# Kernel tuning notes

Hardware: AMD Instinct MI355X
Metric: run time of the kernel (lower is better)

## Reference

```python
import jax, jax.numpy as jnp
import numpy as np

VARIANCES = (0.1, 0.2)
THRESHOLD = 0.35
NEG_POS = 7
NUM_CLASSES = 3
B, P, G = 64, 32768, 64


def point_form(boxes):
    # (cx,cy,w,h) -> (x1,y1,x2,y2)
    return jnp.concatenate([boxes[:, :2] - boxes[:, 2:] / 2,
                            boxes[:, :2] + boxes[:, 2:] / 2], axis=1)


def jaccard(a, b):
    # a: [G,4], b: [P,4], both point-form -> IoU [G,P]
    lt = jnp.maximum(a[:, None, :2], b[None, :, :2])
    rb = jnp.minimum(a[:, None, 2:], b[None, :, 2:])
    wh = jnp.clip(rb - lt, 0.0)
    inter = wh[..., 0] * wh[..., 1]
    area_a = (a[:, 2] - a[:, 0]) * (a[:, 3] - a[:, 1])
    area_b = (b[:, 2] - b[:, 0]) * (b[:, 3] - b[:, 1])
    return inter / (area_a[:, None] + area_b[None, :] - inter)


def encode(matched, priors):
    # matched point-form [P,4], priors center-form [P,4]
    g_cxcy = ((matched[:, :2] + matched[:, 2:]) / 2 - priors[:, :2]) / (VARIANCES[0] * priors[:, 2:])
    g_wh = jnp.log((matched[:, 2:] - matched[:, :2]) / priors[:, 2:]) / VARIANCES[1]
    return jnp.concatenate([g_cxcy, g_wh], axis=1)


def encode_landm(matched, priors):
    # matched [P,10] -> [P,5,2] offsets
    m = matched.reshape(-1, 5, 2)
    g = (m - priors[:, None, :2]) / (VARIANCES[0] * priors[:, None, 2:])
    return g.reshape(-1, 10)


def match_one(truths, labels, landms, priors, priors_pt):
    overlaps = jaccard(truths, priors_pt)                     # [G,P]
    best_prior_overlap = overlaps.max(axis=1)                 # [G]
    best_prior_idx = overlaps.argmax(axis=1)                  # [G]
    valid_gt = best_prior_overlap >= 0.2                      # filter hard gt
    any_valid = valid_gt.any()
    best_truth_overlap = overlaps.max(axis=0)                 # [P]
    best_truth_idx = overlaps.argmax(axis=0)                  # [P]
    # force-match: each valid gt claims its best prior (overlap set to 2 > threshold)
    best_truth_overlap = best_truth_overlap.at[best_prior_idx].max(jnp.where(valid_gt, 2.0, -1.0))
    best_truth_idx = best_truth_idx.at[best_prior_idx].set(jnp.arange(truths.shape[0]))
    matches = truths[best_truth_idx]                          # [P,4]
    conf = labels[best_truth_idx].astype(jnp.int32)           # [P]
    conf = jnp.where(best_truth_overlap < THRESHOLD, 0, conf)
    loc = encode(matches, priors)
    landm = encode_landm(landms[best_truth_idx], priors)
    # early-return branch of match(): no valid gt -> loc_t = 0, conf_t = 0
    loc = jnp.where(any_valid, loc, 0.0)
    conf = jnp.where(any_valid, conf, 0)
    return loc, conf, landm


def smooth_l1(d):
    ad = jnp.abs(d)
    return jnp.where(ad < 1.0, 0.5 * d * d, ad - 0.5)


def setup_inputs() -> dict:
    key = jax.random.key(0)
    k1, k2, k3, k4, k5, k6, k7, k8 = jax.random.split(key, 8)
    loc_data = jax.random.normal(k1, (B, P, 4), dtype=jnp.float32)
    conf_data = jax.random.normal(k2, (B, P, NUM_CLASSES), dtype=jnp.float32)
    landm_data = jax.random.normal(k3, (B, P, 10), dtype=jnp.float32)
    # priors: center-form, in (0,1)
    cxcy = jax.random.uniform(k4, (P, 2), dtype=jnp.float32)
    pwh = jax.random.uniform(k5, (P, 2), dtype=jnp.float32) * 0.28 + 0.02
    priors = jnp.concatenate([cxcy, pwh], axis=1)
    # targets: [B,G,15] = 4 box (point-form) + 10 landm + 1 label in {1,2}
    x1y1 = jax.random.uniform(k6, (B, G, 2), dtype=jnp.float32) * 0.8
    twh = jax.random.uniform(k7, (B, G, 2), dtype=jnp.float32) * 0.18 + 0.02
    lm = jax.random.uniform(k8, (B, G, 10), dtype=jnp.float32)
    lbl = jax.random.randint(jax.random.fold_in(key, 9), (B, G, 1), 1, 3).astype(jnp.float32)
    targets = jnp.concatenate([x1y1, x1y1 + twh, lm, lbl], axis=2)
    return {"loc_data": loc_data, "conf_data": conf_data, "landm_data": landm_data,
            "priors": priors, "targets": targets}


def reference(loc_data, conf_data, landm_data, priors, targets):
    num, num_priors = loc_data.shape[0], priors.shape[0]
    priors_pt = point_form(priors)
    truths, landms, labels = targets[:, :, :4], targets[:, :, 4:14], targets[:, :, 14]
    loc_t, conf_t, landm_t = jax.vmap(match_one, in_axes=(0, 0, 0, None, None))(
        truths, labels, landms, priors, priors_pt)
    loc_t = jax.lax.stop_gradient(loc_t)      # torch builds targets from .data
    landm_t = jax.lax.stop_gradient(landm_t)
    f32 = jnp.float32
    # ---- landmark loss (face: all 10 coords; mask: first 4 coords only) ----
    N1 = jnp.maximum((conf_t > 0).sum().astype(f32), 1.0)
    face = (conf_t == 1)[..., None]
    maskc = (conf_t == 2)[..., None]
    el = smooth_l1(landm_data - landm_t)                      # [B,P,10]
    loss_landm = (el * face).sum() + (el[..., :4] * maskc).sum()
    # ---- localization loss over all positives ----
    pos = conf_t != 0
    loss_l = (smooth_l1(loc_data - loc_t) * pos[..., None]).sum()
    # ---- hard negative mining + confidence loss ----
    conf_t2 = jnp.where(conf_t < 0, 1, conf_t)                # no-landmark faces -> class 1
    lse = jax.nn.logsumexp(conf_data, axis=-1)                # [B,P]
    gathered = jnp.take_along_axis(conf_data, conf_t2[..., None], axis=-1)[..., 0]
    loss_c = jnp.where(pos, 0.0, lse - gathered)              # [B,P]
    loss_idx = jnp.argsort(-loss_c, axis=1)                   # sort descending
    idx_rank = jnp.argsort(loss_idx, axis=1)                  # rank of each prior
    num_pos = pos.sum(axis=1, keepdims=True)
    num_neg = jnp.minimum(NEG_POS * num_pos, num_priors - 1)
    neg = idx_rank < num_neg
    sel = pos | neg
    loss_c_final = jnp.where(sel, lse - gathered, 0.0).sum()
    N = jnp.maximum(num_pos.sum().astype(f32), 1.0)
    return (loss_l / N, loss_c_final / N, loss_landm / N1)
```

## Files before the change

kernel.cpp:

```cpp
#include <hip/hip_runtime.h>

#define B 64
#define P 32768
#define G 64


__device__ __forceinline__ float sl1(float d) {
    float ad = fabsf(d);
    return (ad < 1.0f) ? 0.5f * d * d : (ad - 0.5f);
}

__global__ void k0_init(const float* __restrict__ targets, float* __restrict__ truth_pre,
                        unsigned long long* __restrict__ bp_packed,
                        int* __restrict__ num_pos, int* __restrict__ any_valid,
                        double* __restrict__ acc) {
    int i = blockIdx.x * 256 + threadIdx.x;
    if (i < B * G) {
        const float* t = targets + (size_t)i * 15;
        float x1 = t[0], y1 = t[1], x2 = t[2], y2 = t[3];
        float* o = truth_pre + (size_t)i * 8;
        o[0] = x1; o[1] = y1; o[2] = x2; o[3] = y2;
        o[4] = (x2 - x1) * (y2 - y1); o[5] = t[14]; o[6] = 0.f; o[7] = 0.f;
        bp_packed[i] = 0ull;
    }
    if (i < B) { num_pos[i] = 0; any_valid[i] = 0; }
    if (i < 8) acc[i] = 0.0;
}

__launch_bounds__(256, 8)
__global__ void k1_match(const float* __restrict__ priors, const float* __restrict__ truth_pre,
                         float* __restrict__ bto, int* __restrict__ bti,
                         unsigned long long* __restrict__ bp_packed) {
    __shared__ unsigned long long lbp[G];
    int b = blockIdx.y, tid = threadIdx.x;
    int lane = tid & 63;
    int p = blockIdx.x * 256 + tid;
    int pbase_wave = blockIdx.x * 256 + (tid & ~63);

    float4 pr = ((const float4*)priors)[p];
    float px1 = pr.x - pr.z * 0.5f, py1 = pr.y - pr.w * 0.5f;
    float px2 = pr.x + pr.z * 0.5f, py2 = pr.y + pr.w * 0.5f;
    float pa = (px2 - px1) * (py2 - py1);

    if (tid < G) lbp[tid] = 0ull;
    __syncthreads();

    float bestv = 0.f;
    int bestg = 0;
    const float* tb = truth_pre + (size_t)b * G * 8;

#pragma unroll 4
    for (int g = 0; g < G; ++g) {
        const float* t = tb + g * 8;
        float lx = fmaxf(px1, t[0]);
        float ly = fmaxf(py1, t[1]);
        float rx = fminf(px2, t[2]);
        float ry = fminf(py2, t[3]);
        float w = fmaxf(rx - lx, 0.f), h = fmaxf(ry - ly, 0.f);
        float inter = w * h;
        float denom = (pa + t[4]) - inter;
        float iou = inter * __builtin_amdgcn_rcpf(denom);
        bool better = iou > bestv;
        bestv = better ? iou : bestv;
        bestg = better ? g : bestg;
        float m = iou;
#pragma unroll
        for (int off = 1; off < 64; off <<= 1) m = fmaxf(m, __shfl_xor(m, off));
        unsigned long long msk = __ballot(iou == m);
        int src = __ffsll((long long)msk) - 1;
        unsigned long long pk = ((unsigned long long)__float_as_uint(m) << 32)
                              | (unsigned int)~(unsigned int)(pbase_wave + src);
        if (lane == 0) atomicMax(&lbp[g], pk);
    }
    __syncthreads();
    if (tid < G) atomicMax(&bp_packed[b * G + tid], lbp[tid]);
    bto[(size_t)b * P + p] = bestv;
    bti[(size_t)b * P + p] = bestg;
}

__global__ void k2_force(const unsigned long long* __restrict__ bp_packed,
                         float* __restrict__ bto, int* __restrict__ bti,
                         int* __restrict__ any_valid) {
    int b = blockIdx.x, g = threadIdx.x;
    unsigned long long pk = bp_packed[b * G + g];
    float bpo = __uint_as_float((unsigned int)(pk >> 32));
    unsigned int bpi = ~((unsigned int)pk);
    bool valid = bpo >= 0.2f;
    unsigned long long ball = __ballot(valid);
    if (g == 0) any_valid[b] = (ball != 0ull) ? 1 : 0;
    if (valid) bto[(size_t)b * P + bpi] = 2.0f;
    atomicMax(&bti[(size_t)b * P + bpi], 256 + g);
}

__launch_bounds__(256, 4)
__global__ void k3_loss(const float* __restrict__ loc_data, const float* __restrict__ conf_data,
                        const float* __restrict__ landm_data, const float* __restrict__ priors,
                        const float* __restrict__ targets,
                        const float* __restrict__ bto, const int* __restrict__ bti,
                        const int* __restrict__ any_valid,
                        float* __restrict__ c_neg, int* __restrict__ num_pos,
                        float4* __restrict__ part3) {
    __shared__ float st[G * 15];
    __shared__ float rbuf[12];
    __shared__ int ribuf[4];
    int b = blockIdx.y, tid = threadIdx.x;
    int p = blockIdx.x * 256 + tid;
    for (int i = tid; i < G * 15; i += 256) st[i] = targets[(size_t)b * G * 15 + i];
    __syncthreads();

    size_t idx = (size_t)b * P + p;
    int v = bti[idx];
    int g = (v >= 256) ? (v - 256) : v;
    float ov = bto[idx];
    int conf = 0;
    if (any_valid[b] != 0 && ov >= 0.35f) conf = (int)st[g * 15 + 14];

    const float* cd = conf_data + idx * 3;
    float c0 = cd[0], c1 = cd[1], c2 = cd[2];
    float m = fmaxf(c0, fmaxf(c1, c2));
    float lse = m + __logf(__expf(c0 - m) + __expf(c1 - m) + __expf(c2 - m));
    float gath = (conf == 0) ? c0 : ((conf == 1) ? c1 : c2);
    float lc = lse - gath;

    float cn = 0.f, lloss = 0.f, lmloss = 0.f, plse = 0.f;
    int np = 0;
    if (conf != 0) { np = 1; plse = lc; }
    else cn = fmaxf(lc, 0.f);
    c_neg[idx] = cn;

    if (conf != 0) {
        float4 pr = ((const float4*)priors)[p];
        const float* t = st + g * 15;
        float t0 = t[0], t1 = t[1], t2 = t[2], t3 = t[3];
        float gcx = ((t0 + t2) * 0.5f - pr.x) / (0.1f * pr.z);
        float gcy = ((t1 + t3) * 0.5f - pr.y) / (0.1f * pr.w);
        float gw = __logf((t2 - t0) / pr.z) / 0.2f;
        float gh = __logf((t3 - t1) / pr.w) / 0.2f;
        float4 ld = ((const float4*)loc_data)[idx];
        lloss = sl1(ld.x - gcx) + sl1(ld.y - gcy) + sl1(ld.z - gw) + sl1(ld.w - gh);

        int dims = (conf == 1) ? 10 : 4;
        const float* lmd = landm_data + idx * 10;
        for (int d = 0; d < dims; ++d) {
            float pc = (d & 1) ? pr.y : pr.x;
            float ps = (d & 1) ? pr.w : pr.z;
            float gv = (t[4 + d] - pc) / (0.1f * ps);
            lmloss += sl1(lmd[d] - gv);
        }
    }

    for (int off = 32; off > 0; off >>= 1) {
        lloss  += __shfl_down(lloss, off);
        plse   += __shfl_down(plse, off);
        lmloss += __shfl_down(lmloss, off);
        np     += __shfl_down(np, off);
    }
    int wave = tid >> 6, lane = tid & 63;
    if (lane == 0) { rbuf[wave] = lloss; rbuf[4 + wave] = plse; rbuf[8 + wave] = lmloss; ribuf[wave] = np; }
    __syncthreads();
    if (tid == 0) {
        float a = rbuf[0] + rbuf[1] + rbuf[2] + rbuf[3];
        float bb = rbuf[4] + rbuf[5] + rbuf[6] + rbuf[7];
        float cc = rbuf[8] + rbuf[9] + rbuf[10] + rbuf[11];
        int n = ribuf[0] + ribuf[1] + ribuf[2] + ribuf[3];
        part3[b * gridDim.x + blockIdx.x] = make_float4(a, bb, cc, (float)n);
        if (n) atomicAdd(&num_pos[b], n);
    }
}

__launch_bounds__(1024, 1)
__global__ void k4_mine(const float* __restrict__ c_neg, const int* __restrict__ num_pos,
                        double* __restrict__ acc) {
    __shared__ unsigned int hist[16][256];
    __shared__ unsigned int chist[256];
    __shared__ unsigned int sh_prefix, sh_rem;
    __shared__ double sd[16];
    __shared__ unsigned int sc[16];
    int b = blockIdx.x, tid = threadIdx.x;
    int wv = tid >> 6, lane = tid & 63;
    int npb = num_pos[b];
    long long k = 7LL * npb;
    if (k > P - 1) k = P - 1;
    if (k <= 0) return;
    const float* cb = c_neg + (size_t)b * P;

    unsigned int prefix = 0, remaining = (unsigned int)k;
    for (int byte = 3; byte >= 0; --byte) {
        for (int i = tid; i < 16 * 256; i += 1024) ((unsigned int*)hist)[i] = 0;
        __syncthreads();
        int shift = byte * 8;
        if (byte == 3) {
            for (int i = tid; i < P; i += 1024) {
                unsigned int u = __float_as_uint(cb[i]);
                unsigned int bin = u >> 24;
                unsigned long long todo = __ballot(true);
                while (todo) {
                    int src = (int)(__ffsll((long long)todo) - 1);
                    unsigned int lbin = (unsigned int)__shfl((int)bin, src);
                    unsigned long long mm = __ballot(bin == lbin);
                    if (lane == src) atomicAdd(&hist[wv][lbin], (unsigned int)__popcll(mm));
                    todo &= ~mm;
                }
            }
        } else {
            unsigned int himask = 0xFFFFFFFFu << (shift + 8);
            for (int i = tid; i < P; i += 1024) {
                unsigned int u = __float_as_uint(cb[i]);
                if ((u & himask) == (prefix & himask))
                    atomicAdd(&hist[wv][(u >> shift) & 255u], 1u);
            }
        }
        __syncthreads();
        if (tid < 256) {
            unsigned int s = 0;
#pragma unroll
            for (int w = 0; w < 16; ++w) s += hist[w][tid];
            chist[tid] = s;
        }
        __syncthreads();
        if (wv == 0) {
            int b0 = 255 - 4 * lane;
            unsigned int c0 = chist[b0], c1 = chist[b0 - 1], c2 = chist[b0 - 2], c3 = chist[b0 - 3];
            unsigned int csum = c0 + c1 + c2 + c3;
            unsigned int scan = csum;
            for (int off = 1; off < 64; off <<= 1) {
                unsigned int o = (unsigned int)__shfl_up((int)scan, off);
                if (lane >= off) scan += o;
            }
            unsigned int excl = scan - csum;
            if (scan >= remaining && excl < remaining) {
                int selbin; unsigned int below;
                if (excl + c0 >= remaining)                 { selbin = b0;     below = excl; }
                else if (excl + c0 + c1 >= remaining)       { selbin = b0 - 1; below = excl + c0; }
                else if (excl + c0 + c1 + c2 >= remaining)  { selbin = b0 - 2; below = excl + c0 + c1; }
                else                                        { selbin = b0 - 3; below = excl + c0 + c1 + c2; }
                sh_prefix = prefix | ((unsigned int)selbin << shift);
                sh_rem = remaining - below;
            }
        }
        __syncthreads();
        prefix = sh_prefix; remaining = sh_rem;
        __syncthreads();
    }
    float t = __uint_as_float(prefix);

    double s = 0.0; unsigned int cgt = 0;
    for (int i = tid; i < P; i += 1024) {
        float v = cb[i];
        if (v > t) { s += (double)v; cgt++; }
    }
    for (int off = 32; off > 0; off >>= 1) {
        s += __shfl_down(s, off);
        cgt += __shfl_down(cgt, off);
    }
    if (lane == 0) { sd[wv] = s; sc[wv] = cgt; }
    __syncthreads();
    if (tid == 0) {
        double tot = 0.0; unsigned int cg = 0;
#pragma unroll
        for (int w = 0; w < 16; ++w) { tot += sd[w]; cg += sc[w]; }
        tot += (double)(k - (long long)cg) * (double)t;
        atomicAdd(&acc[1], tot);
    }
}

__global__ void k5_final(const float4* __restrict__ part3, const int* __restrict__ num_pos,
                         const double* __restrict__ acc, float* __restrict__ out,
                         int nparts) {
    __shared__ double sb[3][4];
    int tid = threadIdx.x;
    double sl = 0.0, scn = 0.0, sm = 0.0;
    for (int i = tid; i < nparts; i += 256) {
        float4 v = part3[i];
        sl += (double)v.x; scn += (double)v.y; sm += (double)v.z;
    }
    for (int off = 32; off > 0; off >>= 1) {
        sl += __shfl_down(sl, off);
        scn += __shfl_down(scn, off);
        sm += __shfl_down(sm, off);
    }
    int wave = tid >> 6, lane = tid & 63;
    if (lane == 0) { sb[0][wave] = sl; sb[1][wave] = scn; sb[2][wave] = sm; }
    __syncthreads();
    if (tid == 0) {
        double L = sb[0][0] + sb[0][1] + sb[0][2] + sb[0][3];
        double C = sb[1][0] + sb[1][1] + sb[1][2] + sb[1][3] + acc[1];
        double M = sb[2][0] + sb[2][1] + sb[2][2] + sb[2][3];
        int n = 0;
        for (int i = 0; i < B; ++i) n += num_pos[i];
        double N = (double)(n < 1 ? 1 : n);
        out[0] = (float)(L / N);
        out[1] = (float)(C / N);
        out[2] = (float)(M / N);
    }
}

extern "C" void kernel_launch(void* const* d_in, const int* in_sizes, int n_in,
                              void* d_out, int out_size, void* d_ws, size_t ws_size,
                              hipStream_t stream) {
    const float* loc     = (const float*)d_in[0];
    const float* confd   = (const float*)d_in[1];
    const float* landm   = (const float*)d_in[2];
    const float* priors  = (const float*)d_in[3];
    const float* targets = (const float*)d_in[4];
    float* out = (float*)d_out;

    char* ws = (char*)d_ws;
    double* acc                  = (double*)(ws + 0);
    int* num_pos                 = (int*)(ws + 256);
    int* any_valid               = (int*)(ws + 512);
    unsigned long long* bp       = (unsigned long long*)(ws + 1024);
    float* truth_pre             = (float*)(ws + 33792);
    float4* part3                = (float4*)(ws + 164864);
    float* bto                   = (float*)(ws + 1213440);
    int* bti                     = (int*)(ws + 9602048);
    float* c_neg                 = (float*)(ws + 17990656);

    k0_init<<<dim3((B * G) / 256), dim3(256), 0, stream>>>(targets, truth_pre,
                                                           bp, num_pos, any_valid, acc);
    k1_match<<<dim3(P / 256, B), dim3(256), 0, stream>>>(priors, truth_pre, bto, bti, bp);
    k2_force<<<dim3(B), dim3(64), 0, stream>>>(bp, bto, bti, any_valid);
    k3_loss<<<dim3(P / 256, B), dim3(256), 0, stream>>>(loc, confd, landm, priors, targets,
                                                        bto, bti, any_valid, c_neg, num_pos, part3);
    k4_mine<<<dim3(B), dim3(1024), 0, stream>>>(c_neg, num_pos, acc);
    k5_final<<<1, 256, 0, stream>>>(part3, num_pos, acc, out, (P / 256) * B);
}
```

Measured before the change: 451.2 us.

## Process four priors per thread in match kernel with DPP wave max reduction

Each thread of the matching kernel now handles four contiguous priors. The per-ground-truth wave max reduction is done once per four IoUs, using DPP row operations instead of cross-lane shuffles. Results are written with vectorized float4/int4 stores, and the grid shrinks by four. This cuts reduction and ballot overhead per IoU, at the cost of more registers per thread and fewer blocks in flight.

```diff
diff --git a/kernel.cpp b/kernel.cpp
--- a/kernel.cpp
+++ b/kernel.cpp
@@ -8,6 +8,22 @@
 __device__ __forceinline__ float sl1(float d) {
     float ad = fabsf(d);
     return (ad < 1.0f) ? 0.5f * d * d : (ad - 0.5f);
+}
+
+template <int CTRL>
+__device__ __forceinline__ float dppmax_step(float x) {
+    int xi = __float_as_int(x);
+    int yi = __builtin_amdgcn_update_dpp(xi, xi, CTRL, 0xf, 0xf, false);
+    return fmaxf(x, __int_as_float(yi));
+}
+__device__ __forceinline__ float dppmax64(float v) {
+    float m = dppmax_step<0xB1>(v);
+    m = dppmax_step<0x4E>(m);
+    m = dppmax_step<0x141>(m);
+    m = dppmax_step<0x140>(m);
+    m = dppmax_step<0x142>(m);
+    m = dppmax_step<0x143>(m);
+    return m;
 }
 
 __global__ void k0_init(const float* __restrict__ targets, float* __restrict__ truth_pre,
@@ -27,55 +43,59 @@
     if (i < 8) acc[i] = 0.0;
 }
 
-__launch_bounds__(256, 8)
+__launch_bounds__(256, 4)
 __global__ void k1_match(const float* __restrict__ priors, const float* __restrict__ truth_pre,
                          float* __restrict__ bto, int* __restrict__ bti,
                          unsigned long long* __restrict__ bp_packed) {
     __shared__ unsigned long long lbp[G];
-    int b = blockIdx.y, tid = threadIdx.x;
-    int lane = tid & 63;
-    int p = blockIdx.x * 256 + tid;
-    int pbase_wave = blockIdx.x * 256 + (tid & ~63);
-
-    float4 pr = ((const float4*)priors)[p];
-    float px1 = pr.x - pr.z * 0.5f, py1 = pr.y - pr.w * 0.5f;
-    float px2 = pr.x + pr.z * 0.5f, py2 = pr.y + pr.w * 0.5f;
-    float pa = (px2 - px1) * (py2 - py1);
-
+    const int b = blockIdx.y, tid = threadIdx.x;
+    const int lane = tid & 63;
+    const int p0 = (blockIdx.x * 256 + tid) * 4;
+
+    float px1[4], py1[4], px2[4], py2[4], pa[4], bv[4];
+    int bg[4];
+#pragma unroll
+    for (int k = 0; k < 4; ++k) {
+        float4 pr = ((const float4*)priors)[p0 + k];
+        px1[k] = pr.x - pr.z * 0.5f; py1[k] = pr.y - pr.w * 0.5f;
+        px2[k] = pr.x + pr.z * 0.5f; py2[k] = pr.y + pr.w * 0.5f;
+        pa[k] = (px2[k] - px1[k]) * (py2[k] - py1[k]);
+        bv[k] = 0.f; bg[k] = 0;
+    }
     if (tid < G) lbp[tid] = 0ull;
     __syncthreads();
 
-    float bestv = 0.f;
-    int bestg = 0;
     const float* tb = truth_pre + (size_t)b * G * 8;
-
-#pragma unroll 4
     for (int g = 0; g < G; ++g) {
         const float* t = tb + g * 8;
-        float lx = fmaxf(px1, t[0]);
-        float ly = fmaxf(py1, t[1]);
-        float rx = fminf(px2, t[2]);
-        float ry = fminf(py2, t[3]);
-        float w = fmaxf(rx - lx, 0.f), h = fmaxf(ry - ly, 0.f);
-        float inter = w * h;
-        float denom = (pa + t[4]) - inter;
-        float iou = inter * __builtin_amdgcn_rcpf(denom);
-        bool better = iou > bestv;
-        bestv = better ? iou : bestv;
-        bestg = better ? g : bestg;
-        float m = iou;
+        float t0 = t[0], t1 = t[1], t2 = t[2], t3 = t[3], t4 = t[4];
+        float v = -1.f; int li = 0;
 #pragma unroll
-        for (int off = 1; off < 64; off <<= 1) m = fmaxf(m, __shfl_xor(m, off));
-        unsigned long long msk = __ballot(iou == m);
-        int src = __ffsll((long long)msk) - 1;
-        unsigned long long pk = ((unsigned long long)__float_as_uint(m) << 32)
-                              | (unsigned int)~(unsigned int)(pbase_wave + src);
-        if (lane == 0) atomicMax(&lbp[g], pk);
+        for (int k = 0; k < 4; ++k) {
+            float w = fminf(px2[k], t2) - fmaxf(px1[k], t0);
+            float h = fminf(py2[k], t3) - fmaxf(py1[k], t1);
+            w = fmaxf(w, 0.f); h = fmaxf(h, 0.f);
+            float inter = w * h;
+            float iou = inter * __builtin_amdgcn_rcpf((pa[k] + t4) - inter);
+            if (iou > bv[k]) { bv[k] = iou; bg[k] = g; }
+            if (iou > v) { v = iou; li = k; }
+        }
+        float m = dppmax64(v);
+        float mall = __int_as_float(__builtin_amdgcn_readlane(__float_as_int(m), 63));
+        unsigned long long msk = __ballot(v == mall);
+        int src = (int)__ffsll((long long)msk) - 1;
+        int pwin = __builtin_amdgcn_readlane(p0 + li, src);
+        if (lane == 0) {
+            unsigned long long pk = ((unsigned long long)__float_as_uint(mall) << 32)
+                                  | (unsigned int)~(unsigned int)pwin;
+            atomicMax(&lbp[g], pk);
+        }
     }
     __syncthreads();
     if (tid < G) atomicMax(&bp_packed[b * G + tid], lbp[tid]);
-    bto[(size_t)b * P + p] = bestv;
-    bti[(size_t)b * P + p] = bestg;
+    size_t o = (size_t)b * P + p0;
+    *(float4*)(bto + o) = make_float4(bv[0], bv[1], bv[2], bv[3]);
+    *(int4*)(bti + o)   = make_int4(bg[0], bg[1], bg[2], bg[3]);
 }
 
 __global__ void k2_force(const unsigned long long* __restrict__ bp_packed,
@@ -318,7 +338,7 @@
 
     k0_init<<<dim3((B * G) / 256), dim3(256), 0, stream>>>(targets, truth_pre,
                                                            bp, num_pos, any_valid, acc);
-    k1_match<<<dim3(P / 256, B), dim3(256), 0, stream>>>(priors, truth_pre, bto, bti, bp);
+    k1_match<<<dim3(P / 1024, B), dim3(256), 0, stream>>>(priors, truth_pre, bto, bti, bp);
     k2_force<<<dim3(B), dim3(64), 0, stream>>>(bp, bto, bti, any_valid);
     k3_loss<<<dim3(P / 256, B), dim3(256), 0, stream>>>(loc, confd, landm, priors, targets,
                                                         bto, bti, any_valid, c_neg, num_pos, part3);
```

New measurement: 375.4 us. -16.8%, faster.
